# Optimization experiments

Measured on AMD Instinct MI355X. Metric: run time of the kernel, lower is better.

## Reference

```python
import jax, jax.numpy as jnp
import numpy as np

VOCAB_SIZE = 50257


def setup_inputs() -> dict:
    key = jax.random.key(0)
    B, S = 512, 2048
    assignments = jax.random.randint(key, (B, S), 0, VOCAB_SIZE, dtype=jnp.int64)
    # ones_w are the unit weights scattered into the histogram; counting ones == counting occurrences.
    ones_w = jnp.ones((B, S), dtype=jnp.float32)
    return {"assignments": assignments, "ones_w": ones_w}


def reference(assignments, ones_w):
    # Per-row vocab histogram via scatter-add (avoids the O(B*S*V) broadcast-compare
    # intermediate of the original torch code; same math).
    B, S = assignments.shape
    rows = jnp.arange(B)[:, None]                          # (B, 1) broadcast against (B, S)
    counts = jnp.zeros((B, VOCAB_SIZE), dtype=ones_w.dtype).at[rows, assignments].add(ones_w)
    # Normalize each row's histogram to a frequency distribution.
    frequency = counts / jnp.sum(counts, axis=-1, keepdims=True)
    return frequency
```

## Files before the change

### kernel.cpp

```cpp
#include <hip/hip_runtime.h>

#define VOCAB 50257
#define NCHUNK 4
#define CHUNK ((VOCAB + NCHUNK - 1) / NCHUNK)

__global__ __launch_bounds__(1024) void XTermFrequency_5471788335935_kernel(
    const int* __restrict__ asg, const float* __restrict__ w,
    float* __restrict__ out, int S)
{
    __shared__ float hist[CHUNK];
    __shared__ float s_sum;
    __shared__ float s_inv;

    const int b   = blockIdx.x;
    const int tid = threadIdx.x;
    const long long rowoff = (long long)b * S;
    const int*   __restrict__ row  = asg + rowoff;
    const float* __restrict__ wrow = w   + rowoff;
    float*       __restrict__ orow = out + (long long)b * VOCAB;

    const bool cached = ((S & 1) == 0) && ((S >> 1) == (int)blockDim.x);
    int2   ra = make_int2(0, 0);
    float2 rw = make_float2(0.f, 0.f);
    float  ws = 0.f;
    if (cached) {
        ra = reinterpret_cast<const int2*>(row)[tid];
        rw = reinterpret_cast<const float2*>(wrow)[tid];
        ws = rw.x + rw.y;
    } else {
        for (int s = tid; s < S; s += blockDim.x) ws += wrow[s];
    }

    if (tid == 0) s_sum = 0.f;
    __syncthreads();
    #pragma unroll
    for (int off = 32; off > 0; off >>= 1) ws += __shfl_down(ws, off, 64);
    if ((tid & 63) == 0) atomicAdd(&s_sum, ws);
    __syncthreads();
    if (tid == 0) s_inv = 1.0f / s_sum;

    for (int c = 0; c < NCHUNK; ++c) {
        const int lo = c * CHUNK;

        for (int i = tid; i < CHUNK; i += blockDim.x) hist[i] = 0.f;
        __syncthreads();

        if (cached) {
            const int v0 = ra.x - lo;
            const int v1 = ra.y - lo;
            if ((unsigned)v0 < (unsigned)CHUNK) atomicAdd(&hist[v0], rw.x);
            if ((unsigned)v1 < (unsigned)CHUNK) atomicAdd(&hist[v1], rw.y);
        } else {
            for (int s = tid; s < S; s += blockDim.x) {
                const int v = row[s] - lo;
                if ((unsigned)v < (unsigned)CHUNK) atomicAdd(&hist[v], wrow[s]);
            }
        }
        __syncthreads();

        const float inv = s_inv;
        const int hi = min(CHUNK, VOCAB - lo);
        for (int i = tid; i < hi; i += blockDim.x) orow[lo + i] = hist[i] * inv;
        __syncthreads();
    }
}

extern "C" void kernel_launch(void* const* d_in, const int* in_sizes, int n_in,
                              void* d_out, int out_size, void* d_ws, size_t ws_size,
                              hipStream_t stream) {
    const int*   asg = (const int*)d_in[0];
    const float* w   = (const float*)d_in[1];
    float*       out = (float*)d_out;

    const int B = out_size / VOCAB;
    const int S = in_sizes[0] / B;

    XTermFrequency_5471788335935_kernel<<<B, 1024, 0, stream>>>(asg, w, out, S);
}
```

Measured before the change: 25.29 us.

## Zero-fill output with float4 stores and scatter via global atomics

Drops the four-pass shared-memory chunked histogram. Each block now zero-fills its output row with aligned float4 stores, plus scalar head and tail stores. After one barrier, each element atomically adds its pre-normalized weight straight into global memory. This removes the repeated LDS clearing, the per-chunk barriers and the LDS-to-global copy passes, at the cost of about 2048 global atomics per row and reliance on the barrier ordering the zero stores before the atomics.

```diff
diff --git a/kernel.cpp b/kernel.cpp
--- a/kernel.cpp
+++ b/kernel.cpp
@@ -1,16 +1,12 @@
 #include <hip/hip_runtime.h>
 
 #define VOCAB 50257
-#define NCHUNK 4
-#define CHUNK ((VOCAB + NCHUNK - 1) / NCHUNK)
 
 __global__ __launch_bounds__(1024) void XTermFrequency_5471788335935_kernel(
     const int* __restrict__ asg, const float* __restrict__ w,
     float* __restrict__ out, int S)
 {
-    __shared__ float hist[CHUNK];
     __shared__ float s_sum;
-    __shared__ float s_inv;
 
     const int b   = blockIdx.x;
     const int tid = threadIdx.x;
@@ -36,32 +32,25 @@
     #pragma unroll
     for (int off = 32; off > 0; off >>= 1) ws += __shfl_down(ws, off, 64);
     if ((tid & 63) == 0) atomicAdd(&s_sum, ws);
+
+    const int head = (int)(((16u - ((unsigned)(uintptr_t)orow & 15u)) & 15u) >> 2);
+    if (tid < head) orow[tid] = 0.f;
+    const int nvec = (VOCAB - head) >> 2;
+    float4* __restrict__ vb = reinterpret_cast<float4*>(orow + head);
+    const float4 z4 = make_float4(0.f, 0.f, 0.f, 0.f);
+    for (int i = tid; i < nvec; i += (int)blockDim.x) vb[i] = z4;
+    const int tpos = head + (nvec << 2) + tid;
+    if (tid < 4 && tpos < VOCAB) orow[tpos] = 0.f;
+
     __syncthreads();
-    if (tid == 0) s_inv = 1.0f / s_sum;
 
-    for (int c = 0; c < NCHUNK; ++c) {
-        const int lo = c * CHUNK;
-
-        for (int i = tid; i < CHUNK; i += blockDim.x) hist[i] = 0.f;
-        __syncthreads();
-
-        if (cached) {
-            const int v0 = ra.x - lo;
-            const int v1 = ra.y - lo;
-            if ((unsigned)v0 < (unsigned)CHUNK) atomicAdd(&hist[v0], rw.x);
-            if ((unsigned)v1 < (unsigned)CHUNK) atomicAdd(&hist[v1], rw.y);
-        } else {
-            for (int s = tid; s < S; s += blockDim.x) {
-                const int v = row[s] - lo;
-                if ((unsigned)v < (unsigned)CHUNK) atomicAdd(&hist[v], wrow[s]);
-            }
-        }
-        __syncthreads();
-
-        const float inv = s_inv;
-        const int hi = min(CHUNK, VOCAB - lo);
-        for (int i = tid; i < hi; i += blockDim.x) orow[lo + i] = hist[i] * inv;
-        __syncthreads();
+    const float inv = 1.0f / s_sum;
+    if (cached) {
+        atomicAdd(&orow[ra.x], rw.x * inv);
+        atomicAdd(&orow[ra.y], rw.y * inv);
+    } else {
+        for (int s = tid; s < S; s += blockDim.x)
+            atomicAdd(&orow[row[s]], wrow[s] * inv);
     }
 }
 
```

After: 66.22 us. 2.62x slower.
